# Kernel tuning notes

Hardware: AMD Instinct MI355X
Metric: run time of the kernel (lower is better)

## Reference

```python
import jax, jax.numpy as jnp
import numpy as np

B, D, K, H, L = 8192, 512, 64, 256, 3  # batch, hidden width, rank_k, hypernet hidden, n layers


def _xavier(key, shape):
    fan_in, fan_out = shape[0], shape[1]
    std = float(np.sqrt(2.0 / (fan_in + fan_out)))
    return jax.random.normal(key, shape, dtype=jnp.float32) * std


def setup_inputs() -> dict:
    key = jax.random.key(0)
    ks = jax.random.split(key, 32)
    inp = {"x": jax.random.normal(ks[0], (B, D), dtype=jnp.float32)}
    i = 1
    for l in range(1, L + 1):
        inp[f"U{l}"] = _xavier(ks[i], (D, K)); i += 1
        inp[f"V{l}"] = _xavier(ks[i], (K, D)); i += 1
        # hypernet: cond_dim D -> H -> (K*K + D) [first D cols are bias]
        inp[f"hW1_{l}"] = _xavier(ks[i], (D, H)); i += 1
        inp[f"hb1_{l}"] = jnp.zeros((H,), dtype=jnp.float32)
        inp[f"hW2_{l}"] = _xavier(ks[i], (H, K * K + D)); i += 1
        inp[f"hb2_{l}"] = jnp.zeros((K * K + D,), dtype=jnp.float32)
    inp["Wout"] = _xavier(ks[i], (D, 1)); i += 1
    inp["bout"] = jnp.zeros((1,), dtype=jnp.float32)
    return inp


def _apg_layer(x, U, V, hW1, hb1, hW2, hb2):
    # hypernet (self-wise: condition_z = x)
    h1 = jax.nn.relu(x @ hW1 + hb1)            # [B, H]
    s = h1 @ hW2 + hb2                          # [B, K*K + D]
    bias = s[:, :D]                             # generated per-sample bias [B, D]
    S = s[:, D:].reshape(-1, K, K)              # per-sample weight [B, K, K]
    h = x @ U                                   # [B, K]
    h = jnp.einsum('bk,bkj->bj', h, S)          # bmm(h.unsqueeze(1), S).squeeze(1)
    out = h @ V + bias                          # [B, D]
    return jax.nn.relu(out)


def reference(x,
              U1, V1, hW1_1, hb1_1, hW2_1, hb2_1,
              U2, V2, hW1_2, hb1_2, hW2_2, hb2_2,
              U3, V3, hW1_3, hb1_3, hW2_3, hb2_3,
              Wout, bout):
    x = _apg_layer(x, U1, V1, hW1_1, hb1_1, hW2_1, hb2_1)
    x = _apg_layer(x, U2, V2, hW1_2, hb1_2, hW2_2, hb2_2)
    x = _apg_layer(x, U3, V3, hW1_3, hb1_3, hW2_3, hb2_3)
    return x @ Wout + bout                      # [B, 1]
```

## Files before the change

kernel.cpp:

```cpp
#include <hip/hip_runtime.h>

#define B_N 8192
#define D_N 512
#define K_N 64
#define H_N 256
#define SC  4608
#define R_T 32
#define NT  1024

typedef __attribute__((ext_vector_type(8))) short short8;
typedef __attribute__((ext_vector_type(4))) short short4v;
typedef __attribute__((ext_vector_type(4))) float f32x4;

__device__ __forceinline__ unsigned short f2bf(float f) {
  unsigned int u = __builtin_bit_cast(unsigned int, f);
  u += 0x7fff + ((u >> 16) & 1);
  return (unsigned short)(u >> 16);
}
__device__ __forceinline__ float bf2f(unsigned short h) {
  unsigned int u = ((unsigned int)h) << 16;
  return __builtin_bit_cast(float, u);
}

#define L_ELEMS 1376256

struct PrepParams {
  const float* W1[3]; const float* U[3]; const float* W2[3]; const float* V[3];
  short* ws;
};

__global__ __launch_bounds__(256) void prep_weights(PrepParams p) {
  const int y = blockIdx.y;
  const int l = y / 5, m = y - 5 * l;
  short* wsl = p.ws + (size_t)l * L_ELEMS;
  if (m == 2) {
    const float* in = p.W2[l];
    short* out = wsl + 163840;
    const long total = 1048576;
    for (long e = (long)blockIdx.x * 256 + threadIdx.x; e < total;
         e += (long)gridDim.x * 256) {
      const int te = (int)(e & 7);
      const int j  = (int)((e >> 3) & 63);
      const int tc = (int)((e >> 9) & 31);
      const int kg = (int)(e >> 14);
      const int t  = tc * 8 + te;
      out[e] = (short)f2bf(in[(size_t)t * SC + 512 + 64 * kg + j]);
    }
    return;
  }
  const float* in; short* out; int K, istride, ioff, kshift;
  switch (m) {
    case 0: in = p.W1[l]; out = wsl;           K = 512; istride = 256;  ioff = 0; kshift = 9; break;
    case 1: in = p.U[l];  out = wsl + 131072;  K = 512; istride = 64;   ioff = 0; kshift = 9; break;
    case 3: in = p.W2[l]; out = wsl + 1212416; K = 256; istride = 4608; ioff = 0; kshift = 8; break;
    default:in = p.V[l];  out = wsl + 1343488; K = 64;  istride = 512;  ioff = 0; kshift = 6; break;
  }
  const long total = (long)K * ((m == 0) ? 256 : (m == 1) ? 64 : 512);
  for (long e = (long)blockIdx.x * 256 + threadIdx.x; e < total;
       e += (long)gridDim.x * 256) {
    const int k = (int)(e & (K - 1));
    const int n = (int)(e >> kshift);
    out[e] = (short)f2bf(in[(size_t)k * istride + ioff + n]);
  }
}

struct Params {
  const float* x;
  const float* b1[3];
  const float* b2[3];
  const float* Wout;
  const float* bout;
  const short* ws;
  float* out;
};

#define XP 520
#define HP 264
#define TP 72

__global__ __launch_bounds__(NT, 4) void apg_mfma(Params p) {
  __shared__ short xs[R_T][XP];
  __shared__ short h1s[R_T][HP];
  __shared__ short tmps[R_T][TP];
  __shared__ float hs[R_T][68];
  __shared__ float tpart[4][R_T][68];

  const int tid  = threadIdx.x;
  const int row0 = blockIdx.x * R_T;
  const int w    = tid >> 6;
  const int l15  = tid & 15;
  const int g    = (tid & 63) >> 4;
  const int koff = g * 8;
  const int rh   = w >> 3;
  const int wn   = w & 7;
  const int rbase = rh * 16;

  {
    const float4* xg = (const float4*)(p.x + (size_t)row0 * D_N);
    for (int i = tid; i < R_T * D_N / 4; i += NT) {
      float4 v = xg[i];
      const int r = i >> 7;
      const int c = (i & 127) << 2;
      short4v s4 = { (short)f2bf(v.x), (short)f2bf(v.y), (short)f2bf(v.z), (short)f2bf(v.w) };
      *(short4v*)&xs[r][c] = s4;
    }
  }
  __syncthreads();

  for (int l = 0; l < 3; ++l) {
    const short* wsl  = p.ws + (size_t)l * L_ELEMS;
    const short* W1T  = wsl;
    const short* UT   = wsl + 131072;
    const short* W2p  = wsl + 163840;
    const short* W2bT = wsl + 1212416;
    const short* VT   = wsl + 1343488;
    const float* b1 = p.b1[l];
    const float* b2 = p.b2[l];

    short8 aX[16];
#pragma unroll
    for (int kk = 0; kk < 16; ++kk)
      aX[kk] = *(const short8*)&xs[rbase + l15][kk * 32 + koff];

    for (int nf = 0; nf < 2; ++nf) {
      const int n0 = (wn << 5) + (nf << 4);
      const short* pb = W1T + ((size_t)(n0 + l15) << 9) + koff;
      short8 bf[16];
#pragma unroll
      for (int kk = 0; kk < 16; ++kk) bf[kk] = *(const short8*)(pb + kk * 32);
      f32x4 acc = {0.f, 0.f, 0.f, 0.f};
#pragma unroll
      for (int kk = 0; kk < 16; ++kk)
        acc = __builtin_amdgcn_mfma_f32_16x16x32_bf16(aX[kk], bf[kk], acc, 0, 0, 0);
      const float bb = b1[n0 + l15];
#pragma unroll
      for (int i = 0; i < 4; ++i)
        h1s[rbase + g * 4 + i][n0 + l15] = (short)f2bf(fmaxf(acc[i] + bb, 0.f));
    }

    if (wn < 4) {
      const int n0 = wn << 4;
      const short* pb = UT + ((size_t)(n0 + l15) << 9) + koff;
      short8 bf[16];
#pragma unroll
      for (int kk = 0; kk < 16; ++kk) bf[kk] = *(const short8*)(pb + kk * 32);
      f32x4 acc = {0.f, 0.f, 0.f, 0.f};
#pragma unroll
      for (int kk = 0; kk < 16; ++kk)
        acc = __builtin_amdgcn_mfma_f32_16x16x32_bf16(aX[kk], bf[kk], acc, 0, 0, 0);
#pragma unroll
      for (int i = 0; i < 4; ++i) hs[rbase + g * 4 + i][n0 + l15] = acc[i];
    }
    __syncthreads();

    {
      const int nqc = w & 3;
      const int kq  = (w >> 2) & 3;
      const int kg0 = kq << 4;
      const int nl  = (nqc << 4) + l15;
      short8 aH0[8], aH1[8];
#pragma unroll
      for (int kk = 0; kk < 8; ++kk) {
        aH0[kk] = *(const short8*)&h1s[l15][kk * 32 + koff];
        aH1[kk] = *(const short8*)&h1s[16 + l15][kk * 32 + koff];
      }
      float t0[4] = {0.f, 0.f, 0.f, 0.f}, t1[4] = {0.f, 0.f, 0.f, 0.f};
      {
        const float* pb2 = b2 + D_N + nl;
#pragma unroll 4
        for (int k = kg0; k < kg0 + 16; ++k) {
          const float b2v = pb2[k << 6];
#pragma unroll
          for (int i = 0; i < 4; ++i) {
            t0[i] += hs[g * 4 + i][k] * b2v;
            t1[i] += hs[16 + g * 4 + i][k] * b2v;
          }
        }
      }

      const short* gbase = W2p + (g << 9) + (nl << 3);
      short8 bA[8], bB[8];
      {
        const short* gp = gbase + ((size_t)kg0 << 14);
#pragma unroll
        for (int kk = 0; kk < 8; ++kk) bA[kk] = *(const short8*)(gp + (kk << 11));
      }
#pragma unroll 1
      for (int it = 0; it < 8; ++it) {
        const int kg = kg0 + it * 2;
        {
          const short* gp = gbase + ((size_t)(kg + 1) << 14);
#pragma unroll
          for (int kk = 0; kk < 8; ++kk) bB[kk] = *(const short8*)(gp + (kk << 11));
        }
        {
          f32x4 s0 = {0.f, 0.f, 0.f, 0.f}, s1 = {0.f, 0.f, 0.f, 0.f};
#pragma unroll
          for (int kk = 0; kk < 8; ++kk) {
            s0 = __builtin_amdgcn_mfma_f32_16x16x32_bf16(aH0[kk], bA[kk], s0, 0, 0, 0);
            s1 = __builtin_amdgcn_mfma_f32_16x16x32_bf16(aH1[kk], bA[kk], s1, 0, 0, 0);
          }
#pragma unroll
          for (int i = 0; i < 4; ++i) {
            t0[i] += hs[g * 4 + i][kg] * s0[i];
            t1[i] += hs[16 + g * 4 + i][kg] * s1[i];
          }
        }
        {
          const int kgn = (it == 7) ? (kg + 1) : (kg + 2);
          const short* gp = gbase + ((size_t)kgn << 14);
#pragma unroll
          for (int kk = 0; kk < 8; ++kk) bA[kk] = *(const short8*)(gp + (kk << 11));
        }
        {
          f32x4 s0 = {0.f, 0.f, 0.f, 0.f}, s1 = {0.f, 0.f, 0.f, 0.f};
#pragma unroll
          for (int kk = 0; kk < 8; ++kk) {
            s0 = __builtin_amdgcn_mfma_f32_16x16x32_bf16(aH0[kk], bB[kk], s0, 0, 0, 0);
            s1 = __builtin_amdgcn_mfma_f32_16x16x32_bf16(aH1[kk], bB[kk], s1, 0, 0, 0);
          }
#pragma unroll
          for (int i = 0; i < 4; ++i) {
            t0[i] += hs[g * 4 + i][kg + 1] * s0[i];
            t1[i] += hs[16 + g * 4 + i][kg + 1] * s1[i];
          }
        }
      }

#pragma unroll
      for (int i = 0; i < 4; ++i) {
        tpart[kq][g * 4 + i][nl]      = t0[i];
        tpart[kq][16 + g * 4 + i][nl] = t1[i];
      }
    }
    __syncthreads();

    for (int e = tid; e < R_T * K_N; e += NT) {
      const int r = e >> 6;
      const int c = e & 63;
      const float s = ((tpart[0][r][c] + tpart[1][r][c]) + tpart[2][r][c]) + tpart[3][r][c];
      tmps[r][c] = (short)f2bf(s);
    }
    __syncthreads();

    {
      short8 aT[2], aD[8];
#pragma unroll
      for (int kk = 0; kk < 2; ++kk)
        aT[kk] = *(const short8*)&tmps[rbase + l15][kk * 32 + koff];
#pragma unroll
      for (int kk = 0; kk < 8; ++kk)
        aD[kk] = *(const short8*)&h1s[rbase + l15][kk * 32 + koff];
      for (int ti = 0; ti < 4; ++ti) {
        const int n0 = ((ti << 3) + wn) << 4;
        const short* pv = VT + ((size_t)(n0 + l15) << 6) + koff;
        const short* pw = W2bT + ((size_t)(n0 + l15) << 8) + koff;
        short8 bv[2], bw[8];
#pragma unroll
        for (int kk = 0; kk < 2; ++kk) bv[kk] = *(const short8*)(pv + kk * 32);
#pragma unroll
        for (int kk = 0; kk < 8; ++kk) bw[kk] = *(const short8*)(pw + kk * 32);
        f32x4 acc = {0.f, 0.f, 0.f, 0.f};
#pragma unroll
        for (int kk = 0; kk < 2; ++kk)
          acc = __builtin_amdgcn_mfma_f32_16x16x32_bf16(aT[kk], bv[kk], acc, 0, 0, 0);
#pragma unroll
        for (int kk = 0; kk < 8; ++kk)
          acc = __builtin_amdgcn_mfma_f32_16x16x32_bf16(aD[kk], bw[kk], acc, 0, 0, 0);
        const float bb = b2[n0 + l15];
#pragma unroll
        for (int i = 0; i < 4; ++i)
          xs[rbase + g * 4 + i][n0 + l15] = (short)f2bf(fmaxf(acc[i] + bb, 0.f));
      }
    }
    __syncthreads();
  }

  if (tid < 512) {
    const int r  = tid >> 4;
    const int cl = tid & 15;
    float acc = 0.f;
    for (int c = cl; c < D_N; c += 16)
      acc = fmaf(bf2f((unsigned short)xs[r][c]), p.Wout[c], acc);
#pragma unroll
    for (int s = 1; s < 16; s <<= 1) acc += __shfl_xor(acc, s, 64);
    if (cl == 0) p.out[row0 + r] = acc + p.bout[0];
  }
}

extern "C" void kernel_launch(void* const* d_in, const int* in_sizes, int n_in,
                              void* d_out, int out_size, void* d_ws, size_t ws_size,
                              hipStream_t stream) {
  (void)in_sizes; (void)n_in; (void)ws_size; (void)out_size;
  PrepParams pp;
  Params p;
  p.x = (const float*)d_in[0];
  for (int l = 0; l < 3; ++l) {
    const int base = 1 + l * 6;
    pp.U[l]  = (const float*)d_in[base + 0];
    pp.V[l]  = (const float*)d_in[base + 1];
    pp.W1[l] = (const float*)d_in[base + 2];
    p.b1[l]  = (const float*)d_in[base + 3];
    pp.W2[l] = (const float*)d_in[base + 4];
    p.b2[l]  = (const float*)d_in[base + 5];
  }
  p.Wout = (const float*)d_in[19];
  p.bout = (const float*)d_in[20];
  p.ws   = (const short*)d_ws;
  p.out  = (float*)d_out;
  pp.ws  = (short*)d_ws;

  hipLaunchKernelGGL(prep_weights, dim3(1024, 15), dim3(256), 0, stream, pp);
  hipLaunchKernelGGL(apg_mfma, dim3(B_N / R_T), dim3(NT), 0, stream, p);
}
```

Measured before the change: 228.4 us.

## Cut register pressure and relayout W2 slices for contiguous per-lane loads

Stops holding full A-fragment arrays in registers: activations are read from LDS per MFMA, and the B fragments are loaded in half-K chunks. The per-sample-weight stage now gives each wave one 16-row half and half of the K groups, instead of both row halves and a quarter of K. That halves the accumulators, operand fragments and tpart partial buffers, and shortens the final reduction. The W2 prepack layout is reordered so each lane's eight k-chunks are contiguous (stride 8 shorts rather than 2048). The waves-per-EU attribute pins occupancy at 4. The cost is more LDS reads, and each W2 fragment is now loaded by two waves where one load used to feed both row halves.

```diff
diff --git a/kernel.cpp b/kernel.cpp
--- a/kernel.cpp
+++ b/kernel.cpp
@@ -40,10 +40,11 @@
     for (long e = (long)blockIdx.x * 256 + threadIdx.x; e < total;
          e += (long)gridDim.x * 256) {
       const int te = (int)(e & 7);
-      const int j  = (int)((e >> 3) & 63);
-      const int tc = (int)((e >> 9) & 31);
+      const int kk = (int)((e >> 3) & 7);
+      const int g  = (int)((e >> 6) & 3);
+      const int j  = (int)((e >> 8) & 63);
       const int kg = (int)(e >> 14);
-      const int t  = tc * 8 + te;
+      const int t  = 32 * kk + 8 * g + te;
       out[e] = (short)f2bf(in[(size_t)t * SC + 512 + 64 * kg + j]);
     }
     return;
@@ -78,12 +79,13 @@
 #define HP 264
 #define TP 72
 
-__global__ __launch_bounds__(NT, 4) void apg_mfma(Params p) {
+__global__ __attribute__((amdgpu_waves_per_eu(4, 4)))
+__launch_bounds__(NT) void apg_mfma(Params p) {
   __shared__ short xs[R_T][XP];
   __shared__ short h1s[R_T][HP];
   __shared__ short tmps[R_T][TP];
   __shared__ float hs[R_T][68];
-  __shared__ float tpart[4][R_T][68];
+  __shared__ float tpart[2][R_T][68];
 
   const int tid  = threadIdx.x;
   const int row0 = blockIdx.x * R_T;
@@ -117,21 +119,30 @@
     const float* b1 = p.b1[l];
     const float* b2 = p.b2[l];
 
-    short8 aX[16];
-#pragma unroll
-    for (int kk = 0; kk < 16; ++kk)
-      aX[kk] = *(const short8*)&xs[rbase + l15][kk * 32 + koff];
-
     for (int nf = 0; nf < 2; ++nf) {
       const int n0 = (wn << 5) + (nf << 4);
       const short* pb = W1T + ((size_t)(n0 + l15) << 9) + koff;
-      short8 bf[16];
-#pragma unroll
-      for (int kk = 0; kk < 16; ++kk) bf[kk] = *(const short8*)(pb + kk * 32);
       f32x4 acc = {0.f, 0.f, 0.f, 0.f};
-#pragma unroll
-      for (int kk = 0; kk < 16; ++kk)
-        acc = __builtin_amdgcn_mfma_f32_16x16x32_bf16(aX[kk], bf[kk], acc, 0, 0, 0);
+      {
+        short8 bf[8];
+#pragma unroll
+        for (int kk = 0; kk < 8; ++kk) bf[kk] = *(const short8*)(pb + kk * 32);
+#pragma unroll
+        for (int kk = 0; kk < 8; ++kk) {
+          short8 a = *(const short8*)&xs[rbase + l15][kk * 32 + koff];
+          acc = __builtin_amdgcn_mfma_f32_16x16x32_bf16(a, bf[kk], acc, 0, 0, 0);
+        }
+      }
+      {
+        short8 bf[8];
+#pragma unroll
+        for (int kk = 0; kk < 8; ++kk) bf[kk] = *(const short8*)(pb + 256 + kk * 32);
+#pragma unroll
+        for (int kk = 0; kk < 8; ++kk) {
+          short8 a = *(const short8*)&xs[rbase + l15][256 + kk * 32 + koff];
+          acc = __builtin_amdgcn_mfma_f32_16x16x32_bf16(a, bf[kk], acc, 0, 0, 0);
+        }
+      }
       const float bb = b1[n0 + l15];
 #pragma unroll
       for (int i = 0; i < 4; ++i)
@@ -141,13 +152,27 @@
     if (wn < 4) {
       const int n0 = wn << 4;
       const short* pb = UT + ((size_t)(n0 + l15) << 9) + koff;
-      short8 bf[16];
-#pragma unroll
-      for (int kk = 0; kk < 16; ++kk) bf[kk] = *(const short8*)(pb + kk * 32);
       f32x4 acc = {0.f, 0.f, 0.f, 0.f};
-#pragma unroll
-      for (int kk = 0; kk < 16; ++kk)
-        acc = __builtin_amdgcn_mfma_f32_16x16x32_bf16(aX[kk], bf[kk], acc, 0, 0, 0);
+      {
+        short8 bf[8];
+#pragma unroll
+        for (int kk = 0; kk < 8; ++kk) bf[kk] = *(const short8*)(pb + kk * 32);
+#pragma unroll
+        for (int kk = 0; kk < 8; ++kk) {
+          short8 a = *(const short8*)&xs[rbase + l15][kk * 32 + koff];
+          acc = __builtin_amdgcn_mfma_f32_16x16x32_bf16(a, bf[kk], acc, 0, 0, 0);
+        }
+      }
+      {
+        short8 bf[8];
+#pragma unroll
+        for (int kk = 0; kk < 8; ++kk) bf[kk] = *(const short8*)(pb + 256 + kk * 32);
+#pragma unroll
+        for (int kk = 0; kk < 8; ++kk) {
+          short8 a = *(const short8*)&xs[rbase + l15][256 + kk * 32 + koff];
+          acc = __builtin_amdgcn_mfma_f32_16x16x32_bf16(a, bf[kk], acc, 0, 0, 0);
+        }
+      }
 #pragma unroll
       for (int i = 0; i < 4; ++i) hs[rbase + g * 4 + i][n0 + l15] = acc[i];
     }
@@ -155,118 +180,110 @@
 
     {
       const int nqc = w & 3;
-      const int kq  = (w >> 2) & 3;
-      const int kg0 = kq << 4;
+      const int kh  = (w >> 2) & 1;
+      const int mrh = w >> 3;
+      const int kg0 = kh << 5;
       const int nl  = (nqc << 4) + l15;
-      short8 aH0[8], aH1[8];
-#pragma unroll
-      for (int kk = 0; kk < 8; ++kk) {
-        aH0[kk] = *(const short8*)&h1s[l15][kk * 32 + koff];
-        aH1[kk] = *(const short8*)&h1s[16 + l15][kk * 32 + koff];
-      }
-      float t0[4] = {0.f, 0.f, 0.f, 0.f}, t1[4] = {0.f, 0.f, 0.f, 0.f};
+      const int mb  = mrh << 4;
+      short8 aH[8];
+#pragma unroll
+      for (int kk = 0; kk < 8; ++kk)
+        aH[kk] = *(const short8*)&h1s[mb + l15][kk * 32 + koff];
+
+      float t0[4] = {0.f, 0.f, 0.f, 0.f};
       {
         const float* pb2 = b2 + D_N + nl;
 #pragma unroll 4
-        for (int k = kg0; k < kg0 + 16; ++k) {
+        for (int k = kg0; k < kg0 + 32; ++k) {
           const float b2v = pb2[k << 6];
 #pragma unroll
-          for (int i = 0; i < 4; ++i) {
-            t0[i] += hs[g * 4 + i][k] * b2v;
-            t1[i] += hs[16 + g * 4 + i][k] * b2v;
-          }
-        }
-      }
-
-      const short* gbase = W2p + (g << 9) + (nl << 3);
+          for (int i = 0; i < 4; ++i)
+            t0[i] += hs[mb + g * 4 + i][k] * b2v;
+        }
+      }
+
+      const short* gbase = W2p + ((nl << 2) + g) * 64;
       short8 bA[8], bB[8];
       {
         const short* gp = gbase + ((size_t)kg0 << 14);
 #pragma unroll
-        for (int kk = 0; kk < 8; ++kk) bA[kk] = *(const short8*)(gp + (kk << 11));
+        for (int kk = 0; kk < 8; ++kk) bA[kk] = *(const short8*)(gp + (kk << 3));
       }
 #pragma unroll 1
-      for (int it = 0; it < 8; ++it) {
+      for (int it = 0; it < 16; ++it) {
         const int kg = kg0 + it * 2;
         {
           const short* gp = gbase + ((size_t)(kg + 1) << 14);
 #pragma unroll
-          for (int kk = 0; kk < 8; ++kk) bB[kk] = *(const short8*)(gp + (kk << 11));
-        }
-        {
-          f32x4 s0 = {0.f, 0.f, 0.f, 0.f}, s1 = {0.f, 0.f, 0.f, 0.f};
-#pragma unroll
-          for (int kk = 0; kk < 8; ++kk) {
-            s0 = __builtin_amdgcn_mfma_f32_16x16x32_bf16(aH0[kk], bA[kk], s0, 0, 0, 0);
-            s1 = __builtin_amdgcn_mfma_f32_16x16x32_bf16(aH1[kk], bA[kk], s1, 0, 0, 0);
-          }
-#pragma unroll
-          for (int i = 0; i < 4; ++i) {
-            t0[i] += hs[g * 4 + i][kg] * s0[i];
-            t1[i] += hs[16 + g * 4 + i][kg] * s1[i];
-          }
-        }
-        {
-          const int kgn = (it == 7) ? (kg + 1) : (kg + 2);
+          for (int kk = 0; kk < 8; ++kk) bB[kk] = *(const short8*)(gp + (kk << 3));
+        }
+        {
+          f32x4 s0 = {0.f, 0.f, 0.f, 0.f};
+#pragma unroll
+          for (int kk = 0; kk < 8; ++kk)
+            s0 = __builtin_amdgcn_mfma_f32_16x16x32_bf16(aH[kk], bA[kk], s0, 0, 0, 0);
+#pragma unroll
+          for (int i = 0; i < 4; ++i)
+            t0[i] += hs[mb + g * 4 + i][kg] * s0[i];
+        }
+        {
+          const int kgn = (it == 15) ? (kg + 1) : (kg + 2);
           const short* gp = gbase + ((size_t)kgn << 14);
 #pragma unroll
-          for (int kk = 0; kk < 8; ++kk) bA[kk] = *(const short8*)(gp + (kk << 11));
-        }
-        {
-          f32x4 s0 = {0.f, 0.f, 0.f, 0.f}, s1 = {0.f, 0.f, 0.f, 0.f};
-#pragma unroll
-          for (int kk = 0; kk < 8; ++kk) {
-            s0 = __builtin_amdgcn_mfma_f32_16x16x32_bf16(aH0[kk], bB[kk], s0, 0, 0, 0);
-            s1 = __builtin_amdgcn_mfma_f32_16x16x32_bf16(aH1[kk], bB[kk], s1, 0, 0, 0);
-          }
-#pragma unroll
-          for (int i = 0; i < 4; ++i) {
-            t0[i] += hs[g * 4 + i][kg + 1] * s0[i];
-            t1[i] += hs[16 + g * 4 + i][kg + 1] * s1[i];
-          }
-        }
-      }
-
-#pragma unroll
-      for (int i = 0; i < 4; ++i) {
-        tpart[kq][g * 4 + i][nl]      = t0[i];
-        tpart[kq][16 + g * 4 + i][nl] = t1[i];
-      }
+          for (int kk = 0; kk < 8; ++kk) bA[kk] = *(const short8*)(gp + (kk << 3));
+        }
+        {
+          f32x4 s0 = {0.f, 0.f, 0.f, 0.f};
+#pragma unroll
+          for (int kk = 0; kk < 8; ++kk)
+            s0 = __builtin_amdgcn_mfma_f32_16x16x32_bf16(aH[kk], bB[kk], s0, 0, 0, 0);
+#pragma unroll
+          for (int i = 0; i < 4; ++i)
+            t0[i] += hs[mb + g * 4 + i][kg + 1] * s0[i];
+        }
+      }
+
+#pragma unroll
+      for (int i = 0; i < 4; ++i)
+        tpart[kh][mb + g * 4 + i][nl] = t0[i];
     }
     __syncthreads();
 
     for (int e = tid; e < R_T * K_N; e += NT) {
       const int r = e >> 6;
       const int c = e & 63;
-      const float s = ((tpart[0][r][c] + tpart[1][r][c]) + tpart[2][r][c]) + tpart[3][r][c];
-      tmps[r][c] = (short)f2bf(s);
+      tmps[r][c] = (short)f2bf(tpart[0][r][c] + tpart[1][r][c]);
     }
     __syncthreads();
 
     {
-      short8 aT[2], aD[8];
+      short8 aT[2];
 #pragma unroll
       for (int kk = 0; kk < 2; ++kk)
         aT[kk] = *(const short8*)&tmps[rbase + l15][kk * 32 + koff];
-#pragma unroll
-      for (int kk = 0; kk < 8; ++kk)
-        aD[kk] = *(const short8*)&h1s[rbase + l15][kk * 32 + koff];
       for (int ti = 0; ti < 4; ++ti) {
         const int n0 = ((ti << 3) + wn) << 4;
         const short* pv = VT + ((size_t)(n0 + l15) << 6) + koff;
         const short* pw = W2bT + ((size_t)(n0 + l15) << 8) + koff;
-        short8 bv[2], bw[8];
-#pragma unroll
-        for (int kk = 0; kk < 2; ++kk) bv[kk] = *(const short8*)(pv + kk * 32);
-#pragma unroll
-        for (int kk = 0; kk < 8; ++kk) bw[kk] = *(const short8*)(pw + kk * 32);
         f32x4 acc = {0.f, 0.f, 0.f, 0.f};
-#pragma unroll
-        for (int kk = 0; kk < 2; ++kk)
-          acc = __builtin_amdgcn_mfma_f32_16x16x32_bf16(aT[kk], bv[kk], acc, 0, 0, 0);
-#pragma unroll
-        for (int kk = 0; kk < 8; ++kk)
-          acc = __builtin_amdgcn_mfma_f32_16x16x32_bf16(aD[kk], bw[kk], acc, 0, 0, 0);
+        {
+          short8 bv[2];
+#pragma unroll
+          for (int kk = 0; kk < 2; ++kk) bv[kk] = *(const short8*)(pv + kk * 32);
+#pragma unroll
+          for (int kk = 0; kk < 2; ++kk)
+            acc = __builtin_amdgcn_mfma_f32_16x16x32_bf16(aT[kk], bv[kk], acc, 0, 0, 0);
+        }
+        {
+          short8 bw[8];
+#pragma unroll
+          for (int kk = 0; kk < 8; ++kk) bw[kk] = *(const short8*)(pw + kk * 32);
+#pragma unroll
+          for (int kk = 0; kk < 8; ++kk) {
+            short8 a = *(const short8*)&h1s[rbase + l15][kk * 32 + koff];
+            acc = __builtin_amdgcn_mfma_f32_16x16x32_bf16(a, bw[kk], acc, 0, 0, 0);
+          }
+        }
         const float bb = b2[n0 + l15];
 #pragma unroll
         for (int i = 0; i < 4; ++i)
```

Measured after the change: 534.5 us. 134% more time.
